# Performance work log

Hardware: AMD Instinct MI355X
Metric: run time of the kernel (lower is better)

The kernel has to match this reference:

```python
import jax, jax.numpy as jnp
import numpy as np

B, S, D, H = 2, 2048, 1024, 16
DK = D // H

def setup_inputs() -> dict:
    key = jax.random.key(0)
    ks = jax.random.split(key, 11)
    sc = 1.0 / np.sqrt(D)
    return {
        "q": jax.random.normal(ks[0], (B, S, D), jnp.float32),
        "k": jax.random.normal(ks[1], (B, S, D), jnp.float32),
        "v": jax.random.normal(ks[2], (B, S, D), jnp.float32),
        "Wq": jax.random.normal(ks[3], (D, D), jnp.float32) * sc,
        "bq": jax.random.normal(ks[4], (D,), jnp.float32) * sc,
        "Wk": jax.random.normal(ks[5], (D, D), jnp.float32) * sc,
        "bk": jax.random.normal(ks[6], (D,), jnp.float32) * sc,
        "Wv": jax.random.normal(ks[7], (D, D), jnp.float32) * sc,
        "bv": jax.random.normal(ks[8], (D,), jnp.float32) * sc,
        "Wo": jax.random.normal(ks[9], (D, D), jnp.float32) * sc,
        "bo": jax.random.normal(ks[10], (D,), jnp.float32) * sc,
    }

def reference(q, k, v, Wq, bq, Wk, bk, Wv, bv, Wo, bo):
    b, s, d = q.shape
    # projections (torch Linear: x @ W^T + b)
    qh = (q @ Wq.T + bq).reshape(b, s, H, DK).transpose(0, 2, 1, 3)  # [B,H,S,DK]
    kh = (k @ Wk.T + bk).reshape(b, s, H, DK).transpose(0, 2, 1, 3)
    vh = (v @ Wv.T + bv).reshape(b, s, H, DK).transpose(0, 2, 1, 3)
    scores = jnp.einsum('bhqd,bhkd->bhqk', qh, kh) / jnp.sqrt(jnp.float32(DK))
    attn = jax.nn.softmax(scores, axis=-1)  # [B,H,S,S]
    out = jnp.einsum('bhqk,bhkd->bhqd', attn, vh)  # [B,H,S,DK]
    out = out.transpose(0, 2, 1, 3).reshape(b, s, d)
    return out @ Wo.T + bo
```

## Files before the change

### kernel.cpp

```cpp
#include <hip/hip_runtime.h>
#include <hip/hip_bf16.h>
#include <stdint.h>

typedef __bf16 bf16;
typedef __attribute__((ext_vector_type(8))) __bf16 bf16x8;
typedef __attribute__((ext_vector_type(4))) float f32x4;
typedef __attribute__((ext_vector_type(16))) float f32x16;
typedef __attribute__((ext_vector_type(4))) unsigned int u32x4;
typedef __attribute__((ext_vector_type(2))) unsigned int u32x2;

#define BATCH  2
#define SEQ    2048
#define DMODEL 1024
#define NH     16
#define DKH    64
#define BS     (BATCH*SEQ)
#define BSD    (BS*DMODEL)
#define DD     (DMODEL*DMODEL)

#define QSCALE 0.18033688f

__device__ __forceinline__ void gload_lds16(const bf16* g, bf16* l) {
  __builtin_amdgcn_global_load_lds((const __attribute__((address_space(1))) void*)g,
                                   (__attribute__((address_space(3))) void*)l,
                                   16, 0, 0);
}

__device__ __forceinline__ unsigned int packbf2(float a, float b) {
  union { bf16 h[2]; unsigned int u; } z;
  z.h[0] = (bf16)a; z.h[1] = (bf16)b;
  return z.u;
}

__device__ __forceinline__ float exp2_raw(float x) {
  float r;
  asm("v_exp_f32 %0, %1" : "=v"(r) : "v"(x));
  return r;
}

__device__ __forceinline__ void cvt8(const float* __restrict__ in,
                                     bf16* __restrict__ out, int i) {
  const f32x4* p = (const f32x4*)in + (size_t)i * 2;
  f32x4 a = p[0], b = p[1];
  bf16x8 o;
  o[0]=(bf16)a[0]; o[1]=(bf16)a[1]; o[2]=(bf16)a[2]; o[3]=(bf16)a[3];
  o[4]=(bf16)b[0]; o[5]=(bf16)b[1]; o[6]=(bf16)b[2]; o[7]=(bf16)b[3];
  ((bf16x8*)out)[i] = o;
}

__global__ __launch_bounds__(256) void cvt_all_kernel(
    const float* __restrict__ q, const float* __restrict__ k, const float* __restrict__ v,
    const float* __restrict__ Wq, const float* __restrict__ Wk,
    const float* __restrict__ Wv, const float* __restrict__ Wo,
    bf16* __restrict__ oq, bf16* __restrict__ ok, bf16* __restrict__ ov,
    bf16* __restrict__ oWq, bf16* __restrict__ oWk,
    bf16* __restrict__ oWv, bf16* __restrict__ oWo) {
  int i = blockIdx.x * blockDim.x + threadIdx.x;
  const int z = blockIdx.y;
  if (z == 0)      cvt8(q, oq, i);
  else if (z == 1) cvt8(k, ok, i);
  else if (z == 2) cvt8(v, ov, i);
  else {
    const int w = i >> 17;
    const int j = i & 131071;
    const float* in = (w == 0) ? Wq : (w == 1) ? Wk : (w == 2) ? Wv : Wo;
    bf16* out       = (w == 0) ? oWq : (w == 1) ? oWk : (w == 2) ? oWv : oWo;
    cvt8(in, out, j);
  }
}

template <typename OUT, int MODE, int MR>
__device__ __forceinline__ void gemm_body(const bf16* __restrict__ A,
                                          const bf16* __restrict__ W,
                                          const float* __restrict__ bias,
                                          OUT* __restrict__ C,
                                          float oscale,
                                          bf16* Als, bf16* Bls,
                                          int tx, int ty) {
  const int tid  = threadIdx.x;
  const int lane = tid & 63;
  const int wave = tid >> 6;
  const int wm = wave >> 1, wn = wave & 1;
  const int c = lane & 15, g = lane >> 4;
  const long brow = (long)ty * (MR * 32);
  const long bcol = (long)tx * 128;
  const int  N = DMODEL, K = DMODEL;
  const int  ABUF = MR * 1024;

  f32x4 acc[MR][4] = {};

  const bf16* Ag = A + (brow + wave*16 + ((lane>>2)&15)) * (long)K + (lane & 3) * 8;
  const bf16* Bg = W + (bcol + wave*16 + ((lane>>2)&15)) * (long)K + (lane & 3) * 8;

  auto stage = [&](int kt, int buf) {
    const bf16* a0 = Ag + kt * 32;
    const bf16* b0 = Bg + kt * 32;
    bf16* Ad = Als + buf * ABUF + wave * 512;
    bf16* Bd = Bls + buf * 4096 + wave * 512;
    gload_lds16(a0, Ad);
    if (MR == 4) gload_lds16(a0 + 64 * (long)K, Ad + 2048);
    gload_lds16(b0, Bd);
    gload_lds16(b0 + 64 * (long)K, Bd + 2048);
  };

  const int nk = K >> 5;
  stage(0, 0);
  int cur = 0;
  for (int kt = 0; kt < nk; ++kt) {
    __syncthreads();
    if (kt + 1 < nk) stage(kt + 1, cur ^ 1);

    bf16x8 af[MR], bfv[4];
    #pragma unroll
    for (int m = 0; m < MR; ++m)
      af[m] = *(const bf16x8*)(Als + cur * ABUF + (wm*(MR*16) + m*16 + c) * 32 + g * 8);
    #pragma unroll
    for (int n = 0; n < 4; ++n)
      bfv[n] = *(const bf16x8*)(Bls + cur * 4096 + (wn*64 + n*16 + c) * 32 + g * 8);
    __builtin_amdgcn_s_setprio(1);
    #pragma unroll
    for (int m = 0; m < MR; ++m)
      #pragma unroll
      for (int n = 0; n < 4; ++n)
        acc[m][n] = __builtin_amdgcn_mfma_f32_16x16x32_bf16(af[m], bfv[n], acc[m][n], 0, 0, 0);
    __builtin_amdgcn_s_setprio(0);
    cur ^= 1;
  }

  if (MODE == 0) {
    #pragma unroll
    for (int n = 0; n < 4; ++n) {
      const long col = bcol + wn*64 + n*16 + c;
      const float bb = bias[col];
      #pragma unroll
      for (int m = 0; m < MR; ++m) {
        #pragma unroll
        for (int r = 0; r < 4; ++r) {
          const long row = brow + wm*(MR*16) + m*16 + g*4 + r;
          C[row * (long)N + col] = (OUT)((acc[m][n][r] + bb) * oscale);
        }
      }
    }
  } else {
    const int srow = (int)(brow & (SEQ - 1));
    const int bidx = (int)(brow >> 11);
    #pragma unroll
    for (int n = 0; n < 4; ++n) {
      const int col = (int)bcol + wn*64 + n*16 + c;
      const float bb = bias[col];
      const int h = col >> 6, dk = col & 63;
      OUT* rowp = C + ((size_t)((bidx*16 + h)*64 + dk)) * SEQ + srow + wm*64;
      #pragma unroll
      for (int m = 0; m < MR; ++m) {
        u32x2 pkd;
        pkd[0] = packbf2(acc[m][n][0] + bb, acc[m][n][1] + bb);
        pkd[1] = packbf2(acc[m][n][2] + bb, acc[m][n][3] + bb);
        *(u32x2*)(rowp + m*16 + g*4) = pkd;
      }
    }
  }
}

__global__ __launch_bounds__(256) void gemm_qkv_kernel(
    const bf16* __restrict__ qb, const bf16* __restrict__ kb, const bf16* __restrict__ vb,
    const bf16* __restrict__ Wqb, const bf16* __restrict__ Wkb, const bf16* __restrict__ Wvb,
    const float* __restrict__ bq, const float* __restrict__ bk, const float* __restrict__ bv,
    bf16* __restrict__ qh, bf16* __restrict__ kh, bf16* __restrict__ vt) {
  __shared__ bf16 Als[2 * 128 * 32];
  __shared__ bf16 Bls[2 * 128 * 32];
  const int bid  = blockIdx.x + (blockIdx.y << 3) + (blockIdx.z << 8);
  const int tile = (bid & 7) * 96 + (bid >> 3);
  const int tx = tile & 7, ty = (tile >> 3) & 31, tz = tile >> 8;
  if (tz == 2) {
    gemm_body<bf16, 1, 4>(vb, Wvb, bv, vt, 1.0f, Als, Bls, tx, ty);
  } else {
    const bf16*  A  = (tz == 0) ? qb  : kb;
    const bf16*  W  = (tz == 0) ? Wqb : Wkb;
    const float* bi = (tz == 0) ? bq  : bk;
    bf16*        Cp = (tz == 0) ? qh  : kh;
    const float  os = (tz == 0) ? QSCALE : 1.0f;
    gemm_body<bf16, 0, 4>(A, W, bi, Cp, os, Als, Bls, tx, ty);
  }
}

__global__ __launch_bounds__(256) void gemm_out_kernel(
    const bf16* __restrict__ A, const bf16* __restrict__ Wob,
    const float* __restrict__ bo, float* __restrict__ C) {
  __shared__ bf16 Als[2 * 64 * 32];
  __shared__ bf16 Bls[2 * 128 * 32];
  const int bid  = blockIdx.x + (blockIdx.y << 3);
  const int tile = (bid & 7) * 64 + (bid >> 3);
  const int tx = tile & 7, ty = tile >> 3;
  gemm_body<float, 0, 2>(A, Wob, bo, C, 1.0f, Als, Bls, tx, ty);
}

__global__ __launch_bounds__(512) void attn_kernel(const bf16* __restrict__ qh,
                                                   const bf16* __restrict__ kh,
                                                   const bf16* __restrict__ vt,
                                                   bf16* __restrict__ ao) {
  __shared__ char smem[65536];
  bf16* Kbase = (bf16*)smem;
  bf16* Vbase = (bf16*)(smem + 32768);

  const int tid = threadIdx.x;
  const int lane = tid & 63, wave = tid >> 6;
  const int q32 = lane & 31, hi = lane >> 5;
  const int qg = wave >> 1, half = wave & 1;

  const int bx  = blockIdx.x;
  const int bh  = (bx & 7) * 4 + ((bx >> 3) >> 4);
  const int qt  = (bx >> 3) & 15;
  const int b = bh >> 4, h = bh & 15;
  const long rowbase = (long)b * SEQ;
  const int q0 = qt * 128 + qg * 32;

  const bf16* qp = qh + (rowbase + q0 + q32) * DMODEL + h * 64 + hi * 8;
  bf16x8 qf[4];
  #pragma unroll
  for (int ks = 0; ks < 4; ++ks) qf[ks] = *(const bf16x8*)(qp + ks * 16);

  f32x16 accO0 = {}, accO1 = {};
  f32x16 accL  = {};

  bf16x8 ones8;
  {
    const bf16 sel = (q32 == 0) ? (bf16)1.0f : (bf16)0.0f;
    #pragma unroll
    for (int j = 0; j < 8; ++j) ones8[j] = sel;
  }

  int rd[2][4];
  #pragma unroll
  for (int hh = 0; hh < 2; ++hh) {
    const int row = q32 + 32 * hh;
    const int sw = (row & 7) << 4;
    #pragma unroll
    for (int ks = 0; ks < 4; ++ks)
      rd[hh][ks] = row * 128 + ((ks * 32 + hi * 16) ^ sw);
  }

  const int st_half = tid >> 8;
  const int t8 = tid & 255;
  const int srw = t8 >> 3, stc = t8 & 7;
  const int soff = srw * 128 + ((stc * 16) ^ ((srw & 7) << 4));
  u32x4 kreg0, kreg1, vreg0, vreg1;

  const bf16* kp = kh + (rowbase + st_half * 1024 + srw) * DMODEL + h * 64 + stc * 8;
  const bf16* vp = vt + ((size_t)bh * 64 + srw) * SEQ + st_half * 1024 + stc * 8;

  auto load_tiles = [&]() {
    kreg0 = *(const u32x4*)kp;
    kreg1 = *(const u32x4*)(kp + 32 * DMODEL);
    vreg0 = *(const u32x4*)vp;
    vreg1 = *(const u32x4*)(vp + 32 * SEQ);
    kp += 64 * DMODEL;
    vp += 64;
  };
  auto write_tiles = [&](int buf) {
    char* Kb = (char*)(Kbase + (buf * 2 + st_half) * 4096);
    char* Vb = (char*)(Vbase + (buf * 2 + st_half) * 4096);
    *(u32x4*)(Kb + soff)        = kreg0;
    *(u32x4*)(Kb + soff + 4096) = kreg1;
    *(u32x4*)(Vb + soff)        = vreg0;
    *(u32x4*)(Vb + soff + 4096) = vreg1;
  };

  load_tiles();
  write_tiles(0);
  int cur = 0;
  const int NT2 = SEQ / 64 / 2;

  for (int t = 0; t < NT2; ++t) {
    __syncthreads();
    if (t + 1 < NT2) load_tiles();

    const char* Kb = (const char*)(Kbase + (cur * 2 + half) * 4096);
    const char* Vb = (const char*)(Vbase + (cur * 2 + half) * 4096);

    f32x16 s0 = {}, s1 = {};
    __builtin_amdgcn_s_setprio(1);
    #pragma unroll
    for (int ks = 0; ks < 4; ++ks) {
      bf16x8 k0 = *(const bf16x8*)(Kb + rd[0][ks]);
      s0 = __builtin_amdgcn_mfma_f32_32x32x16_bf16(k0, qf[ks], s0, 0, 0, 0);
    }
    #pragma unroll
    for (int ks = 0; ks < 4; ++ks) {
      bf16x8 k1 = *(const bf16x8*)(Kb + rd[1][ks]);
      s1 = __builtin_amdgcn_mfma_f32_32x32x16_bf16(k1, qf[ks], s1, 0, 0, 0);
    }
    __builtin_amdgcn_s_setprio(0);

    unsigned W0[4][2], W1[4][2];
    #pragma unroll
    for (int t4 = 0; t4 < 4; ++t4) {
      float a0 = exp2_raw(s0[4*t4+0]), a1 = exp2_raw(s0[4*t4+1]);
      float a2 = exp2_raw(s0[4*t4+2]), a3 = exp2_raw(s0[4*t4+3]);
      W0[t4][0] = packbf2(a0, a1); W0[t4][1] = packbf2(a2, a3);
      float b0 = exp2_raw(s1[4*t4+0]), b1 = exp2_raw(s1[4*t4+1]);
      float b2 = exp2_raw(s1[4*t4+2]), b3 = exp2_raw(s1[4*t4+3]);
      W1[t4][0] = packbf2(b0, b1); W1[t4][1] = packbf2(b2, b3);
    }

    bf16x8 Pb[4];
    #pragma unroll
    for (int ks = 0; ks < 4; ++ks) {
      const int t0 = 2 * (ks & 1);
      unsigned w0 = (ks < 2) ? W0[t0][0]     : W1[t0][0];
      unsigned w2 = (ks < 2) ? W0[t0 + 1][0] : W1[t0 + 1][0];
      unsigned w1 = (ks < 2) ? W0[t0][1]     : W1[t0][1];
      unsigned w3 = (ks < 2) ? W0[t0 + 1][1] : W1[t0 + 1][1];
      asm("v_permlane32_swap_b32 %0, %1" : "+v"(w0), "+v"(w2));
      asm("v_permlane32_swap_b32 %0, %1" : "+v"(w1), "+v"(w3));
      union { unsigned u[4]; bf16x8 v; } P;
      P.u[0] = w0; P.u[1] = w1; P.u[2] = w2; P.u[3] = w3;
      Pb[ks] = P.v;
    }

    __builtin_amdgcn_s_setprio(1);
    #pragma unroll
    for (int ks = 0; ks < 4; ++ks) {
      bf16x8 v0 = *(const bf16x8*)(Vb + rd[0][ks]);
      accO0 = __builtin_amdgcn_mfma_f32_32x32x16_bf16(v0, Pb[ks], accO0, 0, 0, 0);
    }
    #pragma unroll
    for (int ks = 0; ks < 4; ++ks) {
      bf16x8 v1 = *(const bf16x8*)(Vb + rd[1][ks]);
      accO1 = __builtin_amdgcn_mfma_f32_32x32x16_bf16(v1, Pb[ks], accO1, 0, 0, 0);
    }
    #pragma unroll
    for (int ks = 0; ks < 4; ++ks)
      accL = __builtin_amdgcn_mfma_f32_32x32x16_bf16(ones8, Pb[ks], accL, 0, 0, 0);
    __builtin_amdgcn_s_setprio(0);

    if (t + 1 < NT2) write_tiles(cur ^ 1);
    cur ^= 1;
  }

  const float lpart = __shfl(accL[0], q32);
  __syncthreads();
  float* cb = (float*)smem + qg * 2176;
  if (half == 1) {
    #pragma unroll
    for (int i = 0; i < 16; ++i) {
      cb[lane + 64 * i]        = accO0[i];
      cb[lane + 64 * (16 + i)] = accO1[i];
    }
    cb[lane + 64 * 32] = lpart;
  }
  __syncthreads();
  if (half == 0) {
    const float lall = lpart + cb[lane + 64 * 32];
    const float inv = 1.f / lall;
    #pragma unroll
    for (int i = 0; i < 16; ++i) {
      accO0[i] += cb[lane + 64 * i];
      accO1[i] += cb[lane + 64 * (16 + i)];
    }
    bf16* dst = ao + (rowbase + q0 + q32) * DMODEL + h * 64;
    #pragma unroll
    for (int t4 = 0; t4 < 4; ++t4) {
      const int d0 = 8 * t4 + 4 * hi;
      u32x2 p0, p1;
      p0[0] = packbf2(accO0[4*t4+0] * inv, accO0[4*t4+1] * inv);
      p0[1] = packbf2(accO0[4*t4+2] * inv, accO0[4*t4+3] * inv);
      *(u32x2*)(dst + d0) = p0;
      p1[0] = packbf2(accO1[4*t4+0] * inv, accO1[4*t4+1] * inv);
      p1[1] = packbf2(accO1[4*t4+2] * inv, accO1[4*t4+3] * inv);
      *(u32x2*)(dst + d0 + 32) = p1;
    }
  }
}

extern "C" void kernel_launch(void* const* d_in, const int* in_sizes, int n_in,
                              void* d_out, int out_size, void* d_ws, size_t ws_size,
                              hipStream_t stream) {
  const float* q  = (const float*)d_in[0];
  const float* k  = (const float*)d_in[1];
  const float* v  = (const float*)d_in[2];
  const float* Wq = (const float*)d_in[3];
  const float* bq = (const float*)d_in[4];
  const float* Wk = (const float*)d_in[5];
  const float* bk = (const float*)d_in[6];
  const float* Wv = (const float*)d_in[7];
  const float* bv = (const float*)d_in[8];
  const float* Wo = (const float*)d_in[9];
  const float* bo = (const float*)d_in[10];
  float* out = (float*)d_out;

  char* w = (char*)d_ws;
  bf16* qb  = (bf16*)w; w += (size_t)BSD * 2;
  bf16* kb  = (bf16*)w; w += (size_t)BSD * 2;
  bf16* vb  = (bf16*)w; w += (size_t)BSD * 2;
  bf16* Wqb = (bf16*)w; w += (size_t)DD * 2;
  bf16* Wkb = (bf16*)w; w += (size_t)DD * 2;
  bf16* Wvb = (bf16*)w; w += (size_t)DD * 2;
  bf16* Wob = (bf16*)w; w += (size_t)DD * 2;
  bf16* qhd = (bf16*)w; w += (size_t)BSD * 2;
  bf16* khd = (bf16*)w; w += (size_t)BSD * 2;
  bf16* vtd = (bf16*)w; w += (size_t)BSD * 2;
  bf16* aod = (bf16*)w; w += (size_t)BSD * 2;

  cvt_all_kernel<<<dim3(BSD / 8 / 256, 4), 256, 0, stream>>>(
      q, k, v, Wq, Wk, Wv, Wo, qb, kb, vb, Wqb, Wkb, Wvb, Wob);

  gemm_qkv_kernel<<<dim3(8, 32, 3), 256, 0, stream>>>(qb, kb, vb, Wqb, Wkb, Wvb,
                                                      bq, bk, bv, qhd, khd, vtd);
  attn_kernel<<<512, 512, 0, stream>>>(qhd, khd, vtd, aod);
  gemm_out_kernel<<<dim3(8, 64), 256, 0, stream>>>(aod, Wob, bo, out);
}
```

Baseline: 124.3 us.

## Fuse fp32-to-bf16 activation conversion into QKV GEMM A-tile staging

```diff
diff --git a/kernel.cpp b/kernel.cpp
--- a/kernel.cpp
+++ b/kernel.cpp
@@ -38,45 +38,32 @@
   return r;
 }
 
-__device__ __forceinline__ void cvt8(const float* __restrict__ in,
-                                     bf16* __restrict__ out, int i) {
-  const f32x4* p = (const f32x4*)in + (size_t)i * 2;
-  f32x4 a = p[0], b = p[1];
-  bf16x8 o;
-  o[0]=(bf16)a[0]; o[1]=(bf16)a[1]; o[2]=(bf16)a[2]; o[3]=(bf16)a[3];
-  o[4]=(bf16)b[0]; o[5]=(bf16)b[1]; o[6]=(bf16)b[2]; o[7]=(bf16)b[3];
-  ((bf16x8*)out)[i] = o;
-}
-
-__global__ __launch_bounds__(256) void cvt_all_kernel(
-    const float* __restrict__ q, const float* __restrict__ k, const float* __restrict__ v,
-    const float* __restrict__ Wq, const float* __restrict__ Wk,
-    const float* __restrict__ Wv, const float* __restrict__ Wo,
-    bf16* __restrict__ oq, bf16* __restrict__ ok, bf16* __restrict__ ov,
-    bf16* __restrict__ oWq, bf16* __restrict__ oWk,
-    bf16* __restrict__ oWv, bf16* __restrict__ oWo) {
+__global__ __launch_bounds__(256) void cvtW_kernel(
+    const float* __restrict__ a, const float* __restrict__ b,
+    const float* __restrict__ c, const float* __restrict__ d,
+    bf16* __restrict__ oa, bf16* __restrict__ ob,
+    bf16* __restrict__ oc, bf16* __restrict__ od) {
   int i = blockIdx.x * blockDim.x + threadIdx.x;
   const int z = blockIdx.y;
-  if (z == 0)      cvt8(q, oq, i);
-  else if (z == 1) cvt8(k, ok, i);
-  else if (z == 2) cvt8(v, ov, i);
-  else {
-    const int w = i >> 17;
-    const int j = i & 131071;
-    const float* in = (w == 0) ? Wq : (w == 1) ? Wk : (w == 2) ? Wv : Wo;
-    bf16* out       = (w == 0) ? oWq : (w == 1) ? oWk : (w == 2) ? oWv : oWo;
-    cvt8(in, out, j);
-  }
-}
-
-template <typename OUT, int MODE, int MR>
-__device__ __forceinline__ void gemm_body(const bf16* __restrict__ A,
+  const float* in = (z == 0) ? a : (z == 1) ? b : (z == 2) ? c : d;
+  bf16* out       = (z == 0) ? oa : (z == 1) ? ob : (z == 2) ? oc : od;
+  const f32x4* p = (const f32x4*)in + (size_t)i * 2;
+  f32x4 x = p[0], y = p[1];
+  bf16x8 o;
+  o[0]=(bf16)x[0]; o[1]=(bf16)x[1]; o[2]=(bf16)x[2]; o[3]=(bf16)x[3];
+  o[4]=(bf16)y[0]; o[5]=(bf16)y[1]; o[6]=(bf16)y[2]; o[7]=(bf16)y[3];
+  ((bf16x8*)out)[i] = o;
+}
+
+template <typename OUT, int MODE, int MR, typename AT>
+__device__ __forceinline__ void gemm_body(const AT* __restrict__ A,
                                           const bf16* __restrict__ W,
                                           const float* __restrict__ bias,
                                           OUT* __restrict__ C,
                                           float oscale,
                                           bf16* Als, bf16* Bls,
                                           int tx, int ty) {
+  constexpr bool AF32 = (sizeof(AT) == 4);
   const int tid  = threadIdx.x;
   const int lane = tid & 63;
   const int wave = tid >> 6;
@@ -89,26 +76,52 @@
 
   f32x4 acc[MR][4] = {};
 
-  const bf16* Ag = A + (brow + wave*16 + ((lane>>2)&15)) * (long)K + (lane & 3) * 8;
+  const AT*   Ag = A + (brow + wave*16 + ((lane>>2)&15)) * (long)K + (lane & 3) * 8;
   const bf16* Bg = W + (bcol + wave*16 + ((lane>>2)&15)) * (long)K + (lane & 3) * 8;
 
-  auto stage = [&](int kt, int buf) {
-    const bf16* a0 = Ag + kt * 32;
+  f32x4 ar[2][2];
+
+  auto stage_issue = [&](int kt, int buf) {
+    if constexpr (AF32) {
+      const float* a0 = (const float*)Ag + kt * 32;
+      ar[0][0] = *(const f32x4*)a0;
+      ar[0][1] = *(const f32x4*)(a0 + 4);
+      const float* a1 = a0 + 64 * (long)K;
+      ar[1][0] = *(const f32x4*)a1;
+      ar[1][1] = *(const f32x4*)(a1 + 4);
+    } else {
+      const bf16* a0 = (const bf16*)Ag + kt * 32;
+      bf16* Ad = Als + buf * ABUF + wave * 512;
+      gload_lds16(a0, Ad);
+      if (MR == 4) gload_lds16(a0 + 64 * (long)K, Ad + 2048);
+    }
     const bf16* b0 = Bg + kt * 32;
-    bf16* Ad = Als + buf * ABUF + wave * 512;
     bf16* Bd = Bls + buf * 4096 + wave * 512;
-    gload_lds16(a0, Ad);
-    if (MR == 4) gload_lds16(a0 + 64 * (long)K, Ad + 2048);
     gload_lds16(b0, Bd);
     gload_lds16(b0 + 64 * (long)K, Bd + 2048);
   };
+  auto stage_writeA = [&](int buf) {
+    if constexpr (AF32) {
+      bf16* Ad = Als + buf * ABUF + wave * 512 + lane * 8;
+      #pragma unroll
+      for (int u = 0; u < 2; ++u) {
+        u32x4 pk;
+        pk[0] = packbf2(ar[u][0][0], ar[u][0][1]);
+        pk[1] = packbf2(ar[u][0][2], ar[u][0][3]);
+        pk[2] = packbf2(ar[u][1][0], ar[u][1][1]);
+        pk[3] = packbf2(ar[u][1][2], ar[u][1][3]);
+        *(u32x4*)(Ad + u * 2048) = pk;
+      }
+    }
+  };
 
   const int nk = K >> 5;
-  stage(0, 0);
+  stage_issue(0, 0);
+  stage_writeA(0);
   int cur = 0;
   for (int kt = 0; kt < nk; ++kt) {
     __syncthreads();
-    if (kt + 1 < nk) stage(kt + 1, cur ^ 1);
+    if (kt + 1 < nk) stage_issue(kt + 1, cur ^ 1);
 
     bf16x8 af[MR], bfv[4];
     #pragma unroll
@@ -124,6 +137,7 @@
       for (int n = 0; n < 4; ++n)
         acc[m][n] = __builtin_amdgcn_mfma_f32_16x16x32_bf16(af[m], bfv[n], acc[m][n], 0, 0, 0);
     __builtin_amdgcn_s_setprio(0);
+    if (kt + 1 < nk) stage_writeA(cur ^ 1);
     cur ^= 1;
   }
 
@@ -162,7 +176,7 @@
 }
 
 __global__ __launch_bounds__(256) void gemm_qkv_kernel(
-    const bf16* __restrict__ qb, const bf16* __restrict__ kb, const bf16* __restrict__ vb,
+    const float* __restrict__ q, const float* __restrict__ k, const float* __restrict__ v,
     const bf16* __restrict__ Wqb, const bf16* __restrict__ Wkb, const bf16* __restrict__ Wvb,
     const float* __restrict__ bq, const float* __restrict__ bk, const float* __restrict__ bv,
     bf16* __restrict__ qh, bf16* __restrict__ kh, bf16* __restrict__ vt) {
@@ -172,14 +186,14 @@
   const int tile = (bid & 7) * 96 + (bid >> 3);
   const int tx = tile & 7, ty = (tile >> 3) & 31, tz = tile >> 8;
   if (tz == 2) {
-    gemm_body<bf16, 1, 4>(vb, Wvb, bv, vt, 1.0f, Als, Bls, tx, ty);
+    gemm_body<bf16, 1, 4, float>(v, Wvb, bv, vt, 1.0f, Als, Bls, tx, ty);
   } else {
-    const bf16*  A  = (tz == 0) ? qb  : kb;
+    const float* A  = (tz == 0) ? q   : k;
     const bf16*  W  = (tz == 0) ? Wqb : Wkb;
     const float* bi = (tz == 0) ? bq  : bk;
     bf16*        Cp = (tz == 0) ? qh  : kh;
     const float  os = (tz == 0) ? QSCALE : 1.0f;
-    gemm_body<bf16, 0, 4>(A, W, bi, Cp, os, Als, Bls, tx, ty);
+    gemm_body<bf16, 0, 4, float>(A, W, bi, Cp, os, Als, Bls, tx, ty);
   }
 }
 
@@ -191,7 +205,7 @@
   const int bid  = blockIdx.x + (blockIdx.y << 3);
   const int tile = (bid & 7) * 64 + (bid >> 3);
   const int tx = tile & 7, ty = tile >> 3;
-  gemm_body<float, 0, 2>(A, Wob, bo, C, 1.0f, Als, Bls, tx, ty);
+  gemm_body<float, 0, 2, bf16>(A, Wob, bo, C, 1.0f, Als, Bls, tx, ty);
 }
 
 __global__ __launch_bounds__(512) void attn_kernel(const bf16* __restrict__ qh,
@@ -389,9 +403,6 @@
   float* out = (float*)d_out;
 
   char* w = (char*)d_ws;
-  bf16* qb  = (bf16*)w; w += (size_t)BSD * 2;
-  bf16* kb  = (bf16*)w; w += (size_t)BSD * 2;
-  bf16* vb  = (bf16*)w; w += (size_t)BSD * 2;
   bf16* Wqb = (bf16*)w; w += (size_t)DD * 2;
   bf16* Wkb = (bf16*)w; w += (size_t)DD * 2;
   bf16* Wvb = (bf16*)w; w += (size_t)DD * 2;
@@ -401,10 +412,10 @@
   bf16* vtd = (bf16*)w; w += (size_t)BSD * 2;
   bf16* aod = (bf16*)w; w += (size_t)BSD * 2;
 
-  cvt_all_kernel<<<dim3(BSD / 8 / 256, 4), 256, 0, stream>>>(
-      q, k, v, Wq, Wk, Wv, Wo, qb, kb, vb, Wqb, Wkb, Wvb, Wob);
-
-  gemm_qkv_kernel<<<dim3(8, 32, 3), 256, 0, stream>>>(qb, kb, vb, Wqb, Wkb, Wvb,
+  cvtW_kernel<<<dim3(DD / 8 / 256, 4), 256, 0, stream>>>(
+      Wq, Wk, Wv, Wo, Wqb, Wkb, Wvb, Wob);
+
+  gemm_qkv_kernel<<<dim3(8, 32, 3), 256, 0, stream>>>(q, k, v, Wqb, Wkb, Wvb,
                                                       bq, bk, bv, qhd, khd, vtd);
   attn_kernel<<<512, 512, 0, stream>>>(qhd, khd, vtd, aod);
   gemm_out_kernel<<<dim3(8, 64), 256, 0, stream>>>(aod, Wob, bo, out);
```

Result: faster. 120.2 us (-3.3%).
